# Optimization experiments

Measured on AMD Instinct MI355X. Metric: run time of the kernel, lower is better.

Reference implementation:

```python
import math
import jax, jax.numpy as jnp
import numpy as np

N_FFT = 1024
HOP = 320
WIN = 800
SR = 32000
N_MELS = 128
FMIN = 0.0
FMAX = SR / 2.0
NUM_BINS = N_FFT // 2 + 1  # 513
PREEMPH = 0.97


def _hann_window(n):
    # torch.hann_window(n, periodic=False): 0.5 - 0.5*cos(2*pi*i/(n-1))
    i = np.arange(n, dtype=np.float64)
    return (0.5 - 0.5 * np.cos(2.0 * np.pi * i / (n - 1))).astype(np.float32)


def _fourier_basis():
    offset = (N_FFT - WIN) // 2
    win_full = np.zeros(N_FFT, dtype=np.float64)
    win_full[offset:offset + WIN] = _hann_window(WIN)
    n = np.arange(N_FFT, dtype=np.float64)[None, :]
    k = np.arange(NUM_BINS, dtype=np.float64)[:, None]
    ang = 2.0 * np.pi * k * (n / float(N_FFT))
    cos_k = np.cos(ang) * win_full
    sin_k = -np.sin(ang) * win_full
    return np.concatenate([cos_k, sin_k], axis=0).astype(np.float32)  # [2*513, 1024]


def _kaldi_mel_banks():
    # torchaudio.compliance.kaldi.get_mel_banks with vtln_warp_factor=1.0
    num_fft_bins = N_FFT // 2
    fft_bin_width = SR / float(N_FFT)
    mel = lambda f: 1127.0 * np.log(1.0 + f / 700.0)
    mel_low, mel_high = mel(FMIN), mel(FMAX)
    delta = (mel_high - mel_low) / (N_MELS + 1)
    left = mel_low + np.arange(N_MELS, dtype=np.float64) * delta  # [M]
    right = left + 2.0 * delta
    freqs = fft_bin_width * np.arange(num_fft_bins, dtype=np.float64)
    m = mel(freqs)[None, :]  # [1, 512]
    up = (m - left[:, None]) / delta
    down = (right[:, None] - m) / delta
    bank = np.maximum(0.0, np.minimum(up, down))  # [128, 512]
    bank = np.pad(bank, ((0, 0), (0, 1)))  # pad one zero column -> [128, 513]
    return bank.astype(np.float32)


def setup_inputs() -> dict:
    key = jax.random.key(0)
    x = jax.random.normal(key, (32, 320000), dtype=jnp.float32)
    return {
        "x": x,
        "fourier_basis": jnp.asarray(_fourier_basis()),
        "mel_basis": jnp.asarray(_kaldi_mel_banks()),
    }


def reference(x, fourier_basis, mel_basis):
    # preemphasis: conv1d with kernel [-0.97, 1.0] (cross-correlation)
    y = x[:, 1:] - PREEMPH * x[:, :-1]  # [B, T-1]
    # center pad by n_fft//2
    pad = N_FFT // 2
    y = jnp.pad(y, ((0, 0), (pad, pad)))
    Tp = y.shape[1]
    frames = (Tp - N_FFT) // HOP + 1
    # frame extraction: [B, frames, n_fft]
    idx = jnp.arange(frames)[:, None] * HOP + jnp.arange(N_FFT)[None, :]
    f = y[:, idx]
    # explicit DFT via dense matmul: [B, 2*num_bins, frames]
    spec = jnp.einsum('btn,cn->bct', f, fourier_basis)
    real = spec[:, :NUM_BINS, :]
    imag = spec[:, NUM_BINS:, :]
    power = real * real + imag * imag  # [B, num_bins, frames]
    mel = jnp.einsum('mf,bft->bmt', mel_basis, power)
    log_mel = (jnp.log(mel + 1e-05) + 4.5) / 5.0
    return log_mel
```

## Files before the change

### kernel.cpp

```cpp
#include <hip/hip_runtime.h>
#include <math.h>

typedef _Float16 half8 __attribute__((ext_vector_type(8)));
typedef float f32x4 __attribute__((ext_vector_type(4)));

constexpr int kNFFT    = 1024;
constexpr int kHop     = 320;
constexpr int kMels    = 128;
constexpr int kFrames  = 1000;
constexpr int kBatch   = 32;
constexpr int kXLen    = 320000;
constexpr int kYLen    = kXLen - 1;
constexpr int kYPad    = 328704;
constexpr int kYOff    = 512;
constexpr float kPre   = 0.97f;
constexpr int kPStride = 544;
constexpr int kKsLo    = 3;
constexpr int kKsHi    = 28;

constexpr size_t kYLvl     = (size_t)kBatch * kYPad;
constexpr size_t kFragLvl  = 64ull * 32 * 64 * 8;
constexpr size_t kFragOff  = 2 * kYLvl;
constexpr size_t kMelFrOff = kFragOff + 2 * kFragLvl;
constexpr size_t kMelFrSz  = 8ull * 17 * 64 * 8;
constexpr size_t kPowOff   = kMelFrOff + kMelFrSz;

constexpr int kYJobBlks   = (kYPad / 8 + 255) / 256;
constexpr int kYJobTotal  = kYJobBlks * kBatch;
constexpr int kFragBlks   = 131072 / 256;
constexpr int kMelBlks    = (8 * 17 * 64) / 256;
constexpr int kPrepGrid   = kYJobTotal + kFragBlks + kMelBlks;

__global__ void prep_all(const float* __restrict__ x, const float* __restrict__ basis,
                         const float* __restrict__ melb, _Float16* __restrict__ ws) {
    _Float16* ypad  = ws;
    _Float16* fr    = ws + kFragOff;
    _Float16* melfr = ws + kMelFrOff;
    const int bid = blockIdx.x;
    const int tid = threadIdx.x;

    if (bid < kYJobTotal) {
        int b = bid / kYJobBlks;
        int blk = bid - b * kYJobBlks;
        int e0 = (blk * 256 + tid) * 8;
        if (e0 >= kYPad) return;
        const float* xb = x + (size_t)b * kXLen;
        int yi = e0 - kYOff;
        float v[8];
        if (yi >= 0 && yi <= kXLen - 9) {
            float4 A = *(const float4*)(xb + yi);
            float4 B = *(const float4*)(xb + yi + 4);
            float C = xb[yi + 8];
            v[0] = A.y - kPre * A.x;  v[1] = A.z - kPre * A.y;
            v[2] = A.w - kPre * A.z;  v[3] = B.x - kPre * A.w;
            v[4] = B.y - kPre * B.x;  v[5] = B.z - kPre * B.y;
            v[6] = B.w - kPre * B.z;  v[7] = C   - kPre * B.w;
        } else {
            #pragma unroll
            for (int j = 0; j < 8; ++j) {
                int g = yi + j;
                v[j] = (g >= 0 && g < kYLen) ? xb[g + 1] - kPre * xb[g] : 0.0f;
            }
        }
        half8 hv, mv;
        #pragma unroll
        for (int j = 0; j < 8; ++j) {
            _Float16 h = (_Float16)v[j];
            hv[j] = h;
            mv[j] = (_Float16)(v[j] - (float)h);
        }
        size_t idx = (size_t)b * kYPad + e0;
        *(half8*)(ypad + idx) = hv;
        *(half8*)(ypad + idx + kYLvl) = mv;
    } else if (bid < kYJobTotal + kFragBlks) {
        int id = (bid - kYJobTotal) * 256 + tid;
        int L  = id & 63;
        int ks = (id >> 6) & 31;
        int g  = id >> 11;
        int r  = 16 * g + (L & 15);
        int orig = (r <= 512) ? r : r + 1;
        const float* src = basis + (size_t)orig * kNFFT + 32 * ks + (L >> 4) * 8;
        float4 s0 = *(const float4*)(src);
        float4 s1 = *(const float4*)(src + 4);
        float a[8] = {s0.x, s0.y, s0.z, s0.w, s1.x, s1.y, s1.z, s1.w};
        half8 hv, mv;
        #pragma unroll
        for (int j = 0; j < 8; ++j) {
            _Float16 h = (_Float16)a[j];
            hv[j] = h;
            mv[j] = (_Float16)(a[j] - (float)h);
        }
        _Float16* dst = fr + (size_t)id * 8;
        *(half8*)dst = hv;
        *(half8*)(dst + kFragLvl) = mv;
    } else {
        int id = (bid - kYJobTotal - kFragBlks) * 256 + tid;
        if (id >= 8 * 17 * 64) return;
        int f = id / 1088;
        int rem = id - f * 1088;
        int ks = rem >> 6;
        int L = rem & 63;
        int m = 16 * f + (L & 15);
        int kb = 32 * ks + (L >> 4) * 8;
        half8 hv;
        #pragma unroll
        for (int j = 0; j < 8; ++j) {
            int k = kb + j;
            hv[j] = (k < 513) ? (_Float16)melb[(size_t)m * 513 + k] : (_Float16)0.0f;
        }
        *(half8*)(melfr + (size_t)id * 8) = hv;
    }
}

__global__ __launch_bounds__(256, 2)
void stft_power(const _Float16* __restrict__ frags,
                const _Float16* __restrict__ ypad,
                _Float16* __restrict__ pw) {
    __shared__ __align__(16) _Float16 ash[2][16 * 512];
    const int tid  = threadIdx.x;
    const int w    = tid >> 6;
    const int lane = tid & 63;
    const int quad = lane >> 4;
    const int l16  = lane & 15;
    const int nt = blockIdx.x, g = blockIdx.y, b = blockIdx.z;
    const int t0 = nt * 256 + w * 64;
    const _Float16* yb0 = ypad + (size_t)b * kYPad;
    const _Float16* yb1 = yb0 + kYLvl;

    f32x4 acc[8][4] = {};

    auto stageA = [&](int ks, int pbuf) {
        #pragma unroll
        for (int c = 0; c < 4; ++c) {
            int slot = w + 4 * c;
            int f = slot & 7, lv = slot >> 3;
            int Gf = (f < 4) ? (4 * g + f) : (32 + 4 * g + (f - 4));
            const _Float16* gp = frags + (size_t)lv * kFragLvl
                               + ((size_t)(Gf * 32 + ks) * 64 + lane) * 8;
            __builtin_amdgcn_global_load_lds(
                (const __attribute__((address_space(1))) void*)gp,
                (__attribute__((address_space(3))) void*)&ash[pbuf][slot * 512],
                16, 0, 0);
        }
    };
    auto loadB2 = [&](int ks, int nf0, half8* bh, half8* bm) {
        #pragma unroll
        for (int nf = nf0; nf < nf0 + 2; ++nf) {
            int off = (t0 + nf * 16 + l16) * kHop + ks * 32 + quad * 8;
            bh[nf] = *(const half8*)(yb0 + off);
            bm[nf] = *(const half8*)(yb1 + off);
        }
    };
    auto mfma2 = [&](int f0, half8 h0, half8 m0, half8 h1, half8 m1,
                     half8* bh, half8* bm) {
        #pragma unroll
        for (int nf = 0; nf < 4; ++nf) {
            f32x4 a = acc[f0][nf];
            a = __builtin_amdgcn_mfma_f32_16x16x32_f16(h0, bh[nf], a, 0, 0, 0);
            a = __builtin_amdgcn_mfma_f32_16x16x32_f16(m0, bh[nf], a, 0, 0, 0);
            a = __builtin_amdgcn_mfma_f32_16x16x32_f16(h0, bm[nf], a, 0, 0, 0);
            acc[f0][nf] = a;
            f32x4 c = acc[f0 + 1][nf];
            c = __builtin_amdgcn_mfma_f32_16x16x32_f16(h1, bh[nf], c, 0, 0, 0);
            c = __builtin_amdgcn_mfma_f32_16x16x32_f16(m1, bh[nf], c, 0, 0, 0);
            c = __builtin_amdgcn_mfma_f32_16x16x32_f16(h1, bm[nf], c, 0, 0, 0);
            acc[f0 + 1][nf] = c;
        }
    };

    auto step = [&](int ks, int pbuf, half8* bhC, half8* bmC,
                    half8* bhN, half8* bmN, bool next) {
        #pragma unroll
        for (int p = 0; p < 4; ++p) {
            const int f0 = 2 * p;
            half8 h0 = *(const half8*)&ash[pbuf][f0 * 512 + lane * 8];
            half8 m0 = *(const half8*)&ash[pbuf][(8 + f0) * 512 + lane * 8];
            half8 h1 = *(const half8*)&ash[pbuf][(f0 + 1) * 512 + lane * 8];
            half8 m1 = *(const half8*)&ash[pbuf][(9 + f0) * 512 + lane * 8];
            if (p == 0 && next) stageA(ks + 1, pbuf ^ 1);
            if (p == 1 && next) loadB2(ks + 1, 0, bhN, bmN);
            if (p == 2 && next) loadB2(ks + 1, 2, bhN, bmN);
            if (p == 3)
                asm volatile("s_waitcnt vmcnt(8)" ::: "memory");
            __builtin_amdgcn_s_barrier();
            __builtin_amdgcn_s_setprio(1);
            mfma2(f0, h0, m0, h1, m1, bhC, bmC);
            __builtin_amdgcn_s_setprio(0);
            __builtin_amdgcn_s_barrier();
        }
    };

    half8 bhA[4], bmA[4], bhB[4], bmB[4];
    stageA(kKsLo, 0);
    loadB2(kKsLo, 0, bhA, bmA);
    loadB2(kKsLo, 2, bhA, bmA);
    asm volatile("s_waitcnt vmcnt(0)" ::: "memory");
    __builtin_amdgcn_s_barrier();

    for (int kss = 0; kss < 13; ++kss) {
        int ks = kKsLo + 2 * kss;
        step(ks,     0, bhA, bmA, bhB, bmB, true);
        step(ks + 1, 1, bhB, bmB, bhA, bmA, kss < 12);
    }

    #pragma unroll
    for (int mf = 0; mf < 4; ++mf) {
        int b0 = 64 * g + 16 * mf + 4 * quad;
        #pragma unroll
        for (int nf = 0; nf < 4; ++nf) {
            int t = t0 + nf * 16 + l16;
            size_t row = ((size_t)((b << 10) + t)) * kPStride;
            struct alignas(8) h4 { _Float16 v[4]; } pp;
            #pragma unroll
            for (int rr = 0; rr < 4; ++rr) {
                float pA = acc[mf][nf][rr];
                float pB = acc[4 + mf][nf][rr];
                float p2 = pA * pA + pB * pB;
                if (g == 0 && mf == 0 && quad == 0 && rr == 0) {
                    p2 = pA * pA;
                    pw[row + 512] = (_Float16)(pB * pB);
                }
                pp.v[rr] = (_Float16)p2;
            }
            *(decltype(pp)*)&pw[row + b0] = pp;
        }
    }
}

__global__ __launch_bounds__(256)
void mel_mfma(const _Float16* __restrict__ melfr, const _Float16* __restrict__ pw,
              float* __restrict__ out) {
    const int tid  = threadIdx.x;
    const int w    = tid >> 6;
    const int lane = tid & 63;
    const int quad = lane >> 4;
    const int l16  = lane & 15;
    const int nt = blockIdx.x, mh = blockIdx.y, b = blockIdx.z;
    const int t = nt * 64 + w * 16 + l16;

    f32x4 acc[4] = {};
    const _Float16* prow = pw + ((size_t)((b << 10) + t)) * kPStride + quad * 8;
    const _Float16* mfr0 = melfr + ((size_t)(mh * 4) * 17 * 64 + lane) * 8;
    #pragma unroll
    for (int ks = 0; ks < 17; ++ks) {
        half8 bp = *(const half8*)(prow + 32 * ks);
        #pragma unroll
        for (int f = 0; f < 4; ++f) {
            half8 af = *(const half8*)(mfr0 + (size_t)(f * 17 + ks) * 64 * 8);
            acc[f] = __builtin_amdgcn_mfma_f32_16x16x32_f16(af, bp, acc[f], 0, 0, 0);
        }
    }
    if (t < kFrames) {
        #pragma unroll
        for (int f = 0; f < 4; ++f) {
            #pragma unroll
            for (int r = 0; r < 4; ++r) {
                int m = mh * 64 + 16 * f + 4 * quad + r;
                out[((size_t)(b * kMels + m)) * kFrames + t] =
                    (__logf(acc[f][r] + 1e-5f) + 4.5f) * 0.2f;
            }
        }
    }
}

extern "C" void kernel_launch(void* const* d_in, const int* in_sizes, int n_in,
                              void* d_out, int out_size, void* d_ws, size_t ws_size,
                              hipStream_t stream) {
    const float* x     = (const float*)d_in[0];
    const float* basis = (const float*)d_in[1];
    const float* melb  = (const float*)d_in[2];
    float* out = (float*)d_out;

    _Float16* ws    = (_Float16*)d_ws;
    _Float16* frags = ws + kFragOff;
    _Float16* melfr = ws + kMelFrOff;
    _Float16* pw    = ws + kPowOff;

    prep_all<<<dim3(kPrepGrid), 256, 0, stream>>>(x, basis, melb, ws);
    stft_power<<<dim3(4, 8, kBatch), 256, 0, stream>>>(frags, ws, pw);
    mel_mfma<<<dim3(16, 2, kBatch), 256, 0, stream>>>(melfr, pw, out);
}
```

Baseline: 240.5 us.

## Load DFT basis fragments directly into registers instead of staging through LDS

Drops the double-buffered shared-memory staging of the Fourier-basis fragments, along with its per-phase barriers and priority hints. Each wave now loads its A fragments straight from global memory into registers and prefetches the next k-step after computing each fragment. This removes the LDS traffic and block-wide synchronisation. In exchange, each of the four waves reads the same basis data separately, which raises global/L2 load traffic and register pressure.

```diff
diff --git a/kernel.cpp b/kernel.cpp
--- a/kernel.cpp
+++ b/kernel.cpp
@@ -116,7 +116,6 @@
 void stft_power(const _Float16* __restrict__ frags,
                 const _Float16* __restrict__ ypad,
                 _Float16* __restrict__ pw) {
-    __shared__ __align__(16) _Float16 ash[2][16 * 512];
     const int tid  = threadIdx.x;
     const int w    = tid >> 6;
     const int lane = tid & 63;
@@ -129,79 +128,47 @@
 
     f32x4 acc[8][4] = {};
 
-    auto stageA = [&](int ks, int pbuf) {
-        #pragma unroll
-        for (int c = 0; c < 4; ++c) {
-            int slot = w + 4 * c;
-            int f = slot & 7, lv = slot >> 3;
-            int Gf = (f < 4) ? (4 * g + f) : (32 + 4 * g + (f - 4));
-            const _Float16* gp = frags + (size_t)lv * kFragLvl
-                               + ((size_t)(Gf * 32 + ks) * 64 + lane) * 8;
-            __builtin_amdgcn_global_load_lds(
-                (const __attribute__((address_space(1))) void*)gp,
-                (__attribute__((address_space(3))) void*)&ash[pbuf][slot * 512],
-                16, 0, 0);
-        }
+    auto loadA1 = [&](int ks, int f, half8& ah_, half8& am_) {
+        int Gf = (f < 4) ? (4 * g + f) : (32 + 4 * g + (f - 4));
+        const _Float16* gp = frags + ((size_t)(Gf * 32 + ks) * 64 + lane) * 8;
+        ah_ = *(const half8*)gp;
+        am_ = *(const half8*)(gp + kFragLvl);
     };
-    auto loadB2 = [&](int ks, int nf0, half8* bh, half8* bm) {
-        #pragma unroll
-        for (int nf = nf0; nf < nf0 + 2; ++nf) {
+    auto loadB = [&](int ks, half8 (&bh)[4], half8 (&bm)[4]) {
+        #pragma unroll
+        for (int nf = 0; nf < 4; ++nf) {
             int off = (t0 + nf * 16 + l16) * kHop + ks * 32 + quad * 8;
             bh[nf] = *(const half8*)(yb0 + off);
             bm[nf] = *(const half8*)(yb1 + off);
         }
     };
-    auto mfma2 = [&](int f0, half8 h0, half8 m0, half8 h1, half8 m1,
-                     half8* bh, half8* bm) {
+    auto computeF = [&](int f, half8 ah_, half8 am_, half8 (&bh)[4], half8 (&bm)[4]) {
         #pragma unroll
         for (int nf = 0; nf < 4; ++nf) {
-            f32x4 a = acc[f0][nf];
-            a = __builtin_amdgcn_mfma_f32_16x16x32_f16(h0, bh[nf], a, 0, 0, 0);
-            a = __builtin_amdgcn_mfma_f32_16x16x32_f16(m0, bh[nf], a, 0, 0, 0);
-            a = __builtin_amdgcn_mfma_f32_16x16x32_f16(h0, bm[nf], a, 0, 0, 0);
-            acc[f0][nf] = a;
-            f32x4 c = acc[f0 + 1][nf];
-            c = __builtin_amdgcn_mfma_f32_16x16x32_f16(h1, bh[nf], c, 0, 0, 0);
-            c = __builtin_amdgcn_mfma_f32_16x16x32_f16(m1, bh[nf], c, 0, 0, 0);
-            c = __builtin_amdgcn_mfma_f32_16x16x32_f16(h1, bm[nf], c, 0, 0, 0);
-            acc[f0 + 1][nf] = c;
+            f32x4 a = acc[f][nf];
+            a = __builtin_amdgcn_mfma_f32_16x16x32_f16(ah_, bh[nf], a, 0, 0, 0);
+            a = __builtin_amdgcn_mfma_f32_16x16x32_f16(am_, bh[nf], a, 0, 0, 0);
+            a = __builtin_amdgcn_mfma_f32_16x16x32_f16(ah_, bm[nf], a, 0, 0, 0);
+            acc[f][nf] = a;
         }
     };
 
-    auto step = [&](int ks, int pbuf, half8* bhC, half8* bmC,
-                    half8* bhN, half8* bmN, bool next) {
-        #pragma unroll
-        for (int p = 0; p < 4; ++p) {
-            const int f0 = 2 * p;
-            half8 h0 = *(const half8*)&ash[pbuf][f0 * 512 + lane * 8];
-            half8 m0 = *(const half8*)&ash[pbuf][(8 + f0) * 512 + lane * 8];
-            half8 h1 = *(const half8*)&ash[pbuf][(f0 + 1) * 512 + lane * 8];
-            half8 m1 = *(const half8*)&ash[pbuf][(9 + f0) * 512 + lane * 8];
-            if (p == 0 && next) stageA(ks + 1, pbuf ^ 1);
-            if (p == 1 && next) loadB2(ks + 1, 0, bhN, bmN);
-            if (p == 2 && next) loadB2(ks + 1, 2, bhN, bmN);
-            if (p == 3)
-                asm volatile("s_waitcnt vmcnt(8)" ::: "memory");
-            __builtin_amdgcn_s_barrier();
-            __builtin_amdgcn_s_setprio(1);
-            mfma2(f0, h0, m0, h1, m1, bhC, bmC);
-            __builtin_amdgcn_s_setprio(0);
-            __builtin_amdgcn_s_barrier();
-        }
-    };
-
-    half8 bhA[4], bmA[4], bhB[4], bmB[4];
-    stageA(kKsLo, 0);
-    loadB2(kKsLo, 0, bhA, bmA);
-    loadB2(kKsLo, 2, bhA, bmA);
-    asm volatile("s_waitcnt vmcnt(0)" ::: "memory");
-    __builtin_amdgcn_s_barrier();
-
-    for (int kss = 0; kss < 13; ++kss) {
-        int ks = kKsLo + 2 * kss;
-        step(ks,     0, bhA, bmA, bhB, bmB, true);
-        step(ks + 1, 1, bhB, bmB, bhA, bmA, kss < 12);
-    }
+    half8 ah[8], am[8], bh[4], bm[4];
+    #pragma unroll
+    for (int f = 0; f < 8; ++f) loadA1(kKsLo, f, ah[f], am[f]);
+    loadB(kKsLo, bh, bm);
+
+    for (int ks = kKsLo; ks < kKsHi; ++ks) {
+        #pragma unroll
+        for (int f = 0; f < 8; ++f) {
+            computeF(f, ah[f], am[f], bh, bm);
+            loadA1(ks + 1, f, ah[f], am[f]);
+        }
+        loadB(ks + 1, bh, bm);
+    }
+    #pragma unroll
+    for (int f = 0; f < 8; ++f)
+        computeF(f, ah[f], am[f], bh, bm);
 
     #pragma unroll
     for (int mf = 0; mf < 4; ++mf) {
```

New measurement: 261.1 us. 1.09x slower.
